# Optimization experiments

Measured on AMD Instinct MI355X. Metric: run time of the kernel, lower is better.

The kernel has to match this reference:

```python
import jax, jax.numpy as jnp
import numpy as np

N_USERS = 1_000_000
N_ITEMS = 100_000
D = 64        # embedding dim
B = 16384     # batch of (user, pos-set, neg-item) triples
S = 20        # size of positive item set


def setup_inputs() -> dict:
    key = jax.random.key(0)
    k1, k2, k3, k4, k5, k6 = jax.random.split(key, 6)
    # original init: (rand - 0.5) * 0.01  -> uniform in (-0.005, 0.005)
    U = (jax.random.uniform(k1, (N_USERS, D), dtype=jnp.float32) - 0.5) * 0.01
    V = (jax.random.uniform(k2, (N_ITEMS, D), dtype=jnp.float32) - 0.5) * 0.01
    bi = jax.random.normal(k3, (N_ITEMS,), dtype=jnp.float32) * 0.01
    user_id = jax.random.randint(k4, (B,), 0, N_USERS, dtype=jnp.int64)
    pos_item_id = jax.random.randint(k5, (B, S), 0, N_ITEMS, dtype=jnp.int64)
    neg_item_id = jax.random.randint(k6, (B,), 0, N_ITEMS, dtype=jnp.int64)
    return {"U": U, "V": V, "bi": bi, "user_id": user_id,
            "pos_item_id": pos_item_id, "neg_item_id": neg_item_id}


def reference(U, V, bi, user_id, pos_item_id, neg_item_id):
    # Fused gather + row-wise dot (replaces diag(matmul) anti-pattern).
    u = U[user_id]                                   # [B, D]
    vp = V[pos_item_id]                              # [B, S, D]
    # caculate_score_pos: mean over the item set of (u . v_i + b_i)
    pos = (jnp.einsum('bd,bsd->bs', u, vp) + bi[pos_item_id]).mean(axis=1)  # [B]
    # caculate_score_neg: u . v_j + b_j
    vn = V[neg_item_id]                              # [B, D]
    neg = jnp.einsum('bd,bd->b', u, vn) + bi[neg_item_id]                   # [B]
    return jnp.stack([pos, neg])                     # [2, B]
```

## Files before the change

### kernel.cpp

```cpp
#include <hip/hip_runtime.h>
#include <hip/hip_bf16.h>


#define DIM 64
#define NPOS 20

__global__ __launch_bounds__(256) void cofiset_kernel(
    const float* __restrict__ U,
    const float* __restrict__ V,
    const float* __restrict__ bi,
    const int*   __restrict__ user_id,
    const int*   __restrict__ pos_item_id,
    const int*   __restrict__ neg_item_id,
    float* __restrict__ out,
    int B)
{
    const int row  = (int)((blockIdx.x * blockDim.x + threadIdx.x) >> 6);
    const int lane = (int)(threadIdx.x & 63);
    if (row >= B) return;

    const int uid = user_id[row];
    const float u = U[(size_t)uid * DIM + lane];

    int   pidx  = 0;
    float pbias = 0.0f;
    if (lane < NPOS) {
        pidx  = pos_item_id[row * NPOS + lane];
        pbias = bi[pidx];
    }

    float accp = pbias;
    #pragma unroll
    for (int s = 0; s < NPOS; ++s) {
        const int idx = __shfl(pidx, s);
        const float v = V[(size_t)idx * DIM + lane];
        accp = fmaf(u, v, accp);
    }

    const int nidx = neg_item_id[row];
    const float vn = V[(size_t)nidx * DIM + lane];
    float accn = u * vn;

    #pragma unroll
    for (int off = 32; off >= 1; off >>= 1) {
        accp += __shfl_xor(accp, off);
        accn += __shfl_xor(accn, off);
    }

    if (lane == 0) {
        out[row]     = accp * (1.0f / (float)NPOS);
        out[B + row] = accn + bi[nidx];
    }
}

extern "C" void kernel_launch(void* const* d_in, const int* in_sizes, int n_in,
                              void* d_out, int out_size, void* d_ws, size_t ws_size,
                              hipStream_t stream) {
    const float* U   = (const float*)d_in[0];
    const float* V   = (const float*)d_in[1];
    const float* bi  = (const float*)d_in[2];
    const int* user_id     = (const int*)d_in[3];
    const int* pos_item_id = (const int*)d_in[4];
    const int* neg_item_id = (const int*)d_in[5];
    float* out = (float*)d_out;

    const int B = in_sizes[3];
    const int rows_per_block = 256 / 64;
    const int grid = (B + rows_per_block - 1) / rows_per_block;

    cofiset_kernel<<<grid, 256, 0, stream>>>(U, V, bi, user_id, pos_item_id,
                                             neg_item_id, out, B);
}
```

Before: 19.22 us.

## Process four rows per wavefront with float4 vectorized gathers

Each 64-lane wavefront now handles four rows, with 16 lanes per row loading float4 slices of the user and item embeddings instead of one float per lane. The positive item indices are spread over two registers so each 16-lane group shuffles its own indices, and the reduction shrinks to four xor steps. The intent is wider memory transactions, fewer shuffle-reduction steps per row, and a quarter of the waves. In exchange each lane issues more dependent FMAs and carries more live registers.

```diff
diff --git a/kernel.cpp b/kernel.cpp
--- a/kernel.cpp
+++ b/kernel.cpp
@@ -15,41 +15,47 @@
     float* __restrict__ out,
     int B)
 {
-    const int row  = (int)((blockIdx.x * blockDim.x + threadIdx.x) >> 6);
-    const int lane = (int)(threadIdx.x & 63);
+    const int gwave = (int)((blockIdx.x * blockDim.x + threadIdx.x) >> 6);
+    const int lane  = (int)(threadIdx.x & 63);
+    const int r     = lane >> 4;
+    const int q     = lane & 15;
+    const int row   = gwave * 4 + r;
     if (row >= B) return;
 
-    const int uid = user_id[row];
-    const float u = U[(size_t)uid * DIM + lane];
+    const int uid  = user_id[row];
+    const int nidx = neg_item_id[row];
+    const int pidx  = pos_item_id[row * NPOS + q];
+    const int pidx2 = (q < 4) ? pos_item_id[row * NPOS + 16 + q] : 0;
 
-    int   pidx  = 0;
-    float pbias = 0.0f;
-    if (lane < NPOS) {
-        pidx  = pos_item_id[row * NPOS + lane];
-        pbias = bi[pidx];
+    const float4 u4 = *(const float4*)&U[(size_t)uid * DIM + q * 4];
+
+    float acc = bi[pidx] + ((q < 4) ? bi[pidx2] : 0.0f);
+    const float nb = bi[nidx];
+
+    const float4 vn = *(const float4*)&V[(size_t)nidx * DIM + q * 4];
+    float accn = u4.x * vn.x + u4.y * vn.y + u4.z * vn.z + u4.w * vn.w;
+
+    const int grp = lane & 48;
+    #pragma unroll
+    for (int s = 0; s < NPOS; ++s) {
+        const int idx = (s < 16) ? __shfl(pidx,  grp + s)
+                                 : __shfl(pidx2, grp + (s - 16));
+        const float4 v4 = *(const float4*)&V[(size_t)idx * DIM + q * 4];
+        acc = fmaf(u4.x, v4.x, acc);
+        acc = fmaf(u4.y, v4.y, acc);
+        acc = fmaf(u4.z, v4.z, acc);
+        acc = fmaf(u4.w, v4.w, acc);
     }
 
-    float accp = pbias;
     #pragma unroll
-    for (int s = 0; s < NPOS; ++s) {
-        const int idx = __shfl(pidx, s);
-        const float v = V[(size_t)idx * DIM + lane];
-        accp = fmaf(u, v, accp);
-    }
-
-    const int nidx = neg_item_id[row];
-    const float vn = V[(size_t)nidx * DIM + lane];
-    float accn = u * vn;
-
-    #pragma unroll
-    for (int off = 32; off >= 1; off >>= 1) {
-        accp += __shfl_xor(accp, off);
+    for (int off = 8; off >= 1; off >>= 1) {
+        acc  += __shfl_xor(acc,  off);
         accn += __shfl_xor(accn, off);
     }
 
-    if (lane == 0) {
-        out[row]     = accp * (1.0f / (float)NPOS);
-        out[B + row] = accn + bi[nidx];
+    if (q == 0) {
+        out[row]     = acc * (1.0f / (float)NPOS);
+        out[B + row] = accn + nb;
     }
 }
 
@@ -65,7 +71,7 @@
     float* out = (float*)d_out;
 
     const int B = in_sizes[3];
-    const int rows_per_block = 256 / 64;
+    const int rows_per_block = 4 * 4;
     const int grid = (B + rows_per_block - 1) / rows_per_block;
 
     cofiset_kernel<<<grid, 256, 0, stream>>>(U, V, bi, user_id, pos_item_id,
```

Result: faster. 18.58 us (-3.3%).
